# Kernel optimization log

Hardware: AMD Instinct MI355X
Metric: run time of the kernel (lower is better)

Reference implementation:

```python
import jax, jax.numpy as jnp
import numpy as np

DIM = 512
HEADS = 8
DIM_HEAD = 64
INNER = HEADS * DIM_HEAD
MAX_POS = 512


def setup_inputs() -> dict:
    key = jax.random.key(0)
    ks = jax.random.split(key, 6)
    b, n = 8, 1024
    x = jax.random.normal(ks[0], (b, n, DIM), dtype=jnp.float32)
    Wq = jax.random.normal(ks[1], (DIM, INNER), dtype=jnp.float32) * (DIM ** -0.5)
    Wkv = jax.random.normal(ks[2], (DIM, 2 * INNER), dtype=jnp.float32) * (DIM ** -0.5)
    rel_emb = jax.random.normal(ks[3], (2 * MAX_POS + 1, DIM_HEAD), dtype=jnp.float32) * 0.02
    Wo = jax.random.normal(ks[4], (INNER, DIM), dtype=jnp.float32) * (INNER ** -0.5)
    bo = jnp.zeros((DIM,), dtype=jnp.float32)
    return {"x": x, "Wq": Wq, "Wkv": Wkv, "rel_emb": rel_emb, "Wo": Wo, "bo": bo}


def reference(x, Wq, Wkv, rel_emb, Wo, bo):
    b, n, _ = x.shape
    scale = DIM_HEAD ** -0.5
    q = x @ Wq                      # [b, n, inner]
    kv = x @ Wkv                    # [b, n, 2*inner]
    k, v = jnp.split(kv, 2, axis=-1)
    # b n (h d) -> b h n d
    split_heads = lambda t: t.reshape(b, n, HEADS, DIM_HEAD).transpose(0, 2, 1, 3)
    q, k, v = split_heads(q), split_heads(k), split_heads(v)
    dots = jnp.einsum('bhid,bhjd->bhij', q, k) * scale  # [b,h,n,n]
    seq = jnp.arange(n)
    dist = jnp.clip(seq[:, None] - seq[None, :], -MAX_POS, MAX_POS) + MAX_POS  # [n,n]
    rel = rel_emb[dist]                                  # [n, n, d]
    pos_attn = jnp.einsum('bhnd,nrd->bhnr', q, rel) * scale
    dots = dots + pos_attn
    attn = jax.nn.softmax(dots, axis=-1)
    out = jnp.einsum('bhij,bhjd->bhid', attn, v)        # [b,h,n,d]
    out = out.transpose(0, 2, 1, 3).reshape(b, n, INNER)
    return out @ Wo + bo
```

## Files before the change

### kernel.cpp

```cpp
#include <hip/hip_runtime.h>

typedef __attribute__((ext_vector_type(8))) short bf16x8;
typedef __attribute__((ext_vector_type(4))) short bf16x4;
typedef __attribute__((ext_vector_type(4))) float f32x4;
typedef unsigned short u16;
typedef unsigned int u32;

#define MFMA16(a, b, c) __builtin_amdgcn_mfma_f32_16x16x32_bf16((a), (b), (c), 0, 0, 0)

__device__ __forceinline__ u16 f2b(float f) {
    u32 u = __float_as_uint(f);
    u32 r = u + 0x7fffu + ((u >> 16) & 1u);
    return (u16)(r >> 16);
}
__device__ __forceinline__ float b2f(u16 u) { return __uint_as_float(((u32)u) << 16); }
__device__ __forceinline__ u32 packbf(float lo, float hi) {
    return (u32)f2b(lo) | ((u32)f2b(hi) << 16);
}

__global__ void k_f32_to_bf16(const float* __restrict__ in, u16* __restrict__ out, int n) {
    int i = (blockIdx.x * blockDim.x + threadIdx.x) * 4;
    if (i + 3 < n) {
        float4 v = *(const float4*)(in + i);
        out[i] = f2b(v.x); out[i + 1] = f2b(v.y); out[i + 2] = f2b(v.z); out[i + 3] = f2b(v.w);
    } else {
        for (int j = i; j < n; ++j) out[j] = f2b(in[j]);
    }
}

__global__ void k_make_wqkv_t(const float* __restrict__ Wq, const float* __restrict__ Wkv,
                              u16* __restrict__ wt) {
    int tid = blockIdx.x * blockDim.x + threadIdx.x;
    int k = tid & 511, n = tid >> 9;
    float v = (n < 512) ? Wq[k * 512 + n] : Wkv[k * 1024 + (n - 512)];
    wt[n * 512 + k] = f2b(v);
}

__global__ void k_make_wo_t(const float* __restrict__ Wo, u16* __restrict__ wt) {
    int tid = blockIdx.x * blockDim.x + threadIdx.x;
    int k = tid & 511, n = tid >> 9;
    wt[n * 512 + k] = f2b(Wo[k * 512 + n]);
}

__global__ __launch_bounds__(256) void k_gemm_qkv(const u16* __restrict__ A, const u16* __restrict__ Bt,
                                                  u16* __restrict__ Q, u16* __restrict__ K,
                                                  u16* __restrict__ V) {
    __shared__ u16 As[128][40];
    __shared__ u16 Bs[128][40];
    const int t = threadIdx.x, l = t & 63, w = t >> 6;
    const int wr = w >> 1, wc = w & 1, l15 = l & 15, lg = l >> 4;
    const int m0 = blockIdx.x * 128, n0 = blockIdx.y * 128;
    f32x4 acc[4][4];
#pragma unroll
    for (int i = 0; i < 4; ++i)
#pragma unroll
        for (int j = 0; j < 4; ++j) acc[i][j] = (f32x4){0.f, 0.f, 0.f, 0.f};
    const int sr = t >> 1, sko = (t & 1) * 16;
    for (int k0 = 0; k0 < 512; k0 += 32) {
        __syncthreads();
        {
            const bf16x8* pa = (const bf16x8*)(A + (size_t)(m0 + sr) * 512 + k0 + sko);
            *(bf16x8*)&As[sr][sko] = pa[0];
            *(bf16x8*)&As[sr][sko + 8] = pa[1];
            const bf16x8* pb = (const bf16x8*)(Bt + (size_t)(n0 + sr) * 512 + k0 + sko);
            *(bf16x8*)&Bs[sr][sko] = pb[0];
            *(bf16x8*)&Bs[sr][sko + 8] = pb[1];
        }
        __syncthreads();
        bf16x8 af[4], bfr[4];
#pragma unroll
        for (int rt = 0; rt < 4; ++rt) af[rt] = *(const bf16x8*)&As[wr * 64 + rt * 16 + l15][lg * 8];
#pragma unroll
        for (int ct = 0; ct < 4; ++ct) bfr[ct] = *(const bf16x8*)&Bs[wc * 64 + ct * 16 + l15][lg * 8];
#pragma unroll
        for (int rt = 0; rt < 4; ++rt)
#pragma unroll
            for (int ct = 0; ct < 4; ++ct) acc[rt][ct] = MFMA16(af[rt], bfr[ct], acc[rt][ct]);
    }
#pragma unroll
    for (int rt = 0; rt < 4; ++rt)
#pragma unroll
        for (int ct = 0; ct < 4; ++ct) {
            int n = n0 + wc * 64 + ct * 16 + l15;
            int sec = n >> 9, nn = n & 511, h = nn >> 6, d = nn & 63;
            u16* dst = (sec == 0) ? Q : ((sec == 1) ? K : V);
#pragma unroll
            for (int r = 0; r < 4; ++r) {
                int m = m0 + wr * 64 + rt * 16 + lg * 4 + r;
                int b = m >> 10, pos = m & 1023, bh = b * 8 + h;
                dst[(size_t)bh * 65536 + (size_t)pos * 64 + d] = f2b(acc[rt][ct][r]);
            }
        }
}

__global__ __launch_bounds__(256) void k_transpose_v(const u16* __restrict__ V, u16* __restrict__ Vt) {
    __shared__ u16 tile[64][72];
    const int bh = blockIdx.x >> 4, pt = blockIdx.x & 15;
    const int p0 = pt * 64;
    const int t = threadIdx.x, r = t >> 2, c0 = (t & 3) * 16;
    const bf16x8* src = (const bf16x8*)(V + (size_t)bh * 65536 + (size_t)(p0 + r) * 64 + c0);
    *(bf16x8*)&tile[r][c0] = src[0];
    *(bf16x8*)&tile[r][c0 + 8] = src[1];
    __syncthreads();
    union { u16 u[8]; bf16x8 v; } o0, o1;
#pragma unroll
    for (int ii = 0; ii < 8; ++ii) {
        o0.u[ii] = tile[c0 + ii][r];
        o1.u[ii] = tile[c0 + 8 + ii][r];
    }
    bf16x8* dst = (bf16x8*)(Vt + (size_t)bh * 65536 + (size_t)r * 1024 + p0 + c0);
    dst[0] = o0.v;
    dst[1] = o1.v;
}

__global__ __launch_bounds__(512, 2) void k_attn(const u16* __restrict__ Q, const u16* __restrict__ K,
                                                 const u16* __restrict__ Vt, const u16* __restrict__ relb,
                                                 u16* __restrict__ Ob) {
    __shared__ u16 Ks[64][72];
    __shared__ u16 Vs[64][72];
    __shared__ u32 sdw[8][16][43];
    const int t = threadIdx.x, l = t & 63, w = t >> 6;
    const int l15 = l & 15, lg = l >> 4;
    const int g = (blockIdx.x & 7) * 64 + (blockIdx.x >> 3);
    const int bh = g >> 3;
    const int iw = (g & 7) * 128 + w * 16;
    const size_t hb = (size_t)bh * 65536;
    const int srow = t >> 3, scol = (t & 7) * 8;

    bf16x8 qf[2];
#pragma unroll
    for (int kf = 0; kf < 2; ++kf)
        qf[kf] = *(const bf16x8*)(Q + hb + (size_t)(iw + l15) * 64 + kf * 32 + lg * 8);

    f32x4 acc_o[4];
#pragma unroll
    for (int i = 0; i < 4; ++i) acc_o[i] = (f32x4){0.f, 0.f, 0.f, 0.f};
    float m_r = -1e30f, l_r = 0.f;

    bf16x8 kreg = *(const bf16x8*)(K + hb + (size_t)srow * 64 + scol);
    bf16x8 vreg = *(const bf16x8*)(Vt + hb + (size_t)srow * 1024 + scol);
    *(bf16x8*)&Ks[srow][scol] = kreg;
    *(bf16x8*)&Vs[srow][scol] = vreg;
    kreg = *(const bf16x8*)(K + hb + (size_t)(64 + srow) * 64 + scol);
    vreg = *(const bf16x8*)(Vt + hb + (size_t)srow * 1024 + 64 + scol);
    __syncthreads();

    for (int j0 = 0; j0 < 1024; j0 += 64) {
        f32x4 acc_s[4];
#pragma unroll
        for (int c = 0; c < 4; ++c) {
            acc_s[c] = (f32x4){0.f, 0.f, 0.f, 0.f};
#pragma unroll
            for (int kf = 0; kf < 2; ++kf) {
                bf16x8 kb = *(const bf16x8*)&Ks[c * 16 + l15][kf * 32 + lg * 8];
                acc_s[c] = MFMA16(kb, qf[kf], acc_s[c]);
            }
        }
        const int bd = iw - j0 - 63;
#pragma unroll
        for (int pt = 0; pt < 5; ++pt) {
            int dd = bd + pt * 16 + l15;
            dd = dd < -512 ? -512 : (dd > 512 ? 512 : dd);
            const u16* rrow = relb + (size_t)(dd + 512) * 64;
            f32x4 a = (f32x4){0.f, 0.f, 0.f, 0.f};
#pragma unroll
            for (int kf = 0; kf < 2; ++kf) {
                bf16x8 rb = *(const bf16x8*)(rrow + kf * 32 + lg * 8);
                a = MFMA16(rb, qf[kf], a);
            }
            int wc32 = pt * 8 + lg * 2;
            sdw[w][l15][wc32] = packbf(a[0], a[1]);
            sdw[w][l15][wc32 + 1] = packbf(a[2], a[3]);
        }
        asm volatile("s_waitcnt lgkmcnt(0)" ::: "memory");
        __builtin_amdgcn_sched_barrier(0);
        float sv[4][4];
#pragma unroll
        for (int c = 0; c < 4; ++c)
#pragma unroll
            for (int r = 0; r < 4; ++r) {
                int tt = l15 + 63 - c * 16 - lg * 4 - r;
                u32 wv = sdw[w][l15][tt >> 1];
                float band = b2f((u16)(wv >> ((tt & 1) * 16)));
                sv[c][r] = (acc_s[c][r] + band) * 0.125f;
            }
        float mt = sv[0][0];
#pragma unroll
        for (int c = 0; c < 4; ++c)
#pragma unroll
            for (int r = 0; r < 4; ++r) mt = fmaxf(mt, sv[c][r]);
        mt = fmaxf(mt, __shfl_xor(mt, 16, 64));
        mt = fmaxf(mt, __shfl_xor(mt, 32, 64));
        float mnew = fmaxf(m_r, mt);
        float alpha = __expf(m_r - mnew);
        m_r = mnew;
        float p[4][4];
        float rs = 0.f;
#pragma unroll
        for (int c = 0; c < 4; ++c)
#pragma unroll
            for (int r = 0; r < 4; ++r) {
                p[c][r] = __expf(sv[c][r] - mnew);
                rs += p[c][r];
            }
        rs += __shfl_xor(rs, 16, 64);
        rs += __shfl_xor(rs, 32, 64);
        l_r = l_r * alpha + rs;
#pragma unroll
        for (int dt = 0; dt < 4; ++dt)
#pragma unroll
            for (int r = 0; r < 4; ++r) acc_o[dt][r] *= alpha;
        union { u32 wd[4]; bf16x8 v; } pb[2];
#pragma unroll
        for (int kf = 0; kf < 2; ++kf)
#pragma unroll
            for (int h = 0; h < 4; ++h) {
                int c = kf * 2 + (h >> 1), r0 = (h & 1) * 2;
                pb[kf].wd[h] = packbf(p[c][r0], p[c][r0 + 1]);
            }
#pragma unroll
        for (int dt = 0; dt < 4; ++dt)
#pragma unroll
            for (int kf = 0; kf < 2; ++kf) {
                union { bf16x4 h[2]; bf16x8 v; } vb;
                vb.h[0] = *(const bf16x4*)&Vs[dt * 16 + l15][kf * 32 + lg * 4];
                vb.h[1] = *(const bf16x4*)&Vs[dt * 16 + l15][kf * 32 + 16 + lg * 4];
                acc_o[dt] = MFMA16(vb.v, pb[kf].v, acc_o[dt]);
            }
        __syncthreads();
        if (j0 + 64 < 1024) {
            *(bf16x8*)&Ks[srow][scol] = kreg;
            *(bf16x8*)&Vs[srow][scol] = vreg;
            int jp = j0 / 64 + 2;
            if (jp > 15) jp = 15;
            kreg = *(const bf16x8*)(K + hb + (size_t)(jp * 64 + srow) * 64 + scol);
            vreg = *(const bf16x8*)(Vt + hb + (size_t)srow * 1024 + jp * 64 + scol);
            __syncthreads();
        }
    }
    const int b = bh >> 3, h = bh & 7;
    const float rinv = 1.0f / l_r;
    const size_t rowbase = (size_t)(b * 1024 + iw + l15) * 512 + h * 64;
#pragma unroll
    for (int dt = 0; dt < 4; ++dt)
#pragma unroll
        for (int hp = 0; hp < 2; ++hp) {
            u32 pkd = packbf(acc_o[dt][hp * 2] * rinv, acc_o[dt][hp * 2 + 1] * rinv);
            *(u32*)(Ob + rowbase + dt * 16 + lg * 4 + hp * 2) = pkd;
        }
}

__global__ __launch_bounds__(256) void k_gemm_out(const u16* __restrict__ A, const u16* __restrict__ Bt,
                                                  const float* __restrict__ bias, float* __restrict__ out) {
    __shared__ u16 As[128][40];
    __shared__ u16 Bs[128][40];
    const int t = threadIdx.x, l = t & 63, w = t >> 6;
    const int wr = w >> 1, wc = w & 1, l15 = l & 15, lg = l >> 4;
    const int m0 = blockIdx.x * 128, n0 = blockIdx.y * 128;
    f32x4 acc[4][4];
#pragma unroll
    for (int i = 0; i < 4; ++i)
#pragma unroll
        for (int j = 0; j < 4; ++j) acc[i][j] = (f32x4){0.f, 0.f, 0.f, 0.f};
    const int sr = t >> 1, sko = (t & 1) * 16;
    for (int k0 = 0; k0 < 512; k0 += 32) {
        __syncthreads();
        {
            const bf16x8* pa = (const bf16x8*)(A + (size_t)(m0 + sr) * 512 + k0 + sko);
            *(bf16x8*)&As[sr][sko] = pa[0];
            *(bf16x8*)&As[sr][sko + 8] = pa[1];
            const bf16x8* pb = (const bf16x8*)(Bt + (size_t)(n0 + sr) * 512 + k0 + sko);
            *(bf16x8*)&Bs[sr][sko] = pb[0];
            *(bf16x8*)&Bs[sr][sko + 8] = pb[1];
        }
        __syncthreads();
        bf16x8 af[4], bfr[4];
#pragma unroll
        for (int rt = 0; rt < 4; ++rt) af[rt] = *(const bf16x8*)&As[wr * 64 + rt * 16 + l15][lg * 8];
#pragma unroll
        for (int ct = 0; ct < 4; ++ct) bfr[ct] = *(const bf16x8*)&Bs[wc * 64 + ct * 16 + l15][lg * 8];
#pragma unroll
        for (int rt = 0; rt < 4; ++rt)
#pragma unroll
            for (int ct = 0; ct < 4; ++ct) acc[rt][ct] = MFMA16(af[rt], bfr[ct], acc[rt][ct]);
    }
#pragma unroll
    for (int rt = 0; rt < 4; ++rt)
#pragma unroll
        for (int ct = 0; ct < 4; ++ct) {
            int n = n0 + wc * 64 + ct * 16 + l15;
            float bv = bias[n];
#pragma unroll
            for (int r = 0; r < 4; ++r) {
                int m = m0 + wr * 64 + rt * 16 + lg * 4 + r;
                out[(size_t)m * 512 + n] = acc[rt][ct][r] + bv;
            }
        }
}

extern "C" void kernel_launch(void* const* d_in, const int* in_sizes, int n_in,
                              void* d_out, int out_size, void* d_ws, size_t ws_size,
                              hipStream_t stream) {
    const float* x    = (const float*)d_in[0];
    const float* Wq   = (const float*)d_in[1];
    const float* Wkv  = (const float*)d_in[2];
    const float* rel  = (const float*)d_in[3];
    const float* Wo   = (const float*)d_in[4];
    const float* bo   = (const float*)d_in[5];
    float* out = (float*)d_out;
    char* ws = (char*)d_ws;

    u16* xb   = (u16*)(ws + 0);
    u16* wqkv = (u16*)(ws + 8388608);
    u16* wot  = (u16*)(ws + 9961472);
    u16* relb = (u16*)(ws + 10485760);
    u16* Q    = (u16*)(ws + 10616960);
    u16* K    = (u16*)(ws + 19005568);
    u16* V    = (u16*)(ws + 27394176);
    u16* Vt   = (u16*)(ws + 35782784);
    u16* Ob   = (u16*)(ws + 44171392);

    k_f32_to_bf16<<<4096, 256, 0, stream>>>(x, xb, 4194304);
    k_f32_to_bf16<<<65, 256, 0, stream>>>(rel, relb, 65600);
    k_make_wqkv_t<<<3072, 256, 0, stream>>>(Wq, Wkv, wqkv);
    k_make_wo_t<<<1024, 256, 0, stream>>>(Wo, wot);
    k_gemm_qkv<<<dim3(64, 12), 256, 0, stream>>>(xb, wqkv, Q, K, V);
    k_transpose_v<<<1024, 256, 0, stream>>>(V, Vt);
    k_attn<<<512, 512, 0, stream>>>(Q, K, Vt, relb, Ob);
    k_gemm_out<<<dim3(64, 4), 256, 0, stream>>>(Ob, wot, bo, out);
}
```

Before: 150.5 us.

## Split attention KV range in two with flash-decoding style combine kernel

Each attention block now processes only half of the key sequence, doubling the grid from 512 to 1024 blocks. Each block writes fp16 partial outputs plus per-row max and sum. A new combine kernel merges the two halves into the bf16 output layout. This targets low occupancy and load imbalance on the 256-CU device (512 blocks at 2 per CU), at the cost of extra partial-output traffic, an extra launch, and reuse of workspace buffers for the partials.

Result: slower. 188.7 us (+25.4%).

```diff
diff --git a/kernel.cpp b/kernel.cpp
--- a/kernel.cpp
+++ b/kernel.cpp
@@ -1,4 +1,5 @@
 #include <hip/hip_runtime.h>
+#include <hip/hip_fp16.h>
 
 typedef __attribute__((ext_vector_type(8))) short bf16x8;
 typedef __attribute__((ext_vector_type(4))) short bf16x4;
@@ -17,6 +18,10 @@
 __device__ __forceinline__ u32 packbf(float lo, float hi) {
     return (u32)f2b(lo) | ((u32)f2b(hi) << 16);
 }
+__device__ __forceinline__ u32 packh(float lo, float hi) {
+    return (u32)__half_as_ushort(__float2half(lo)) | ((u32)__half_as_ushort(__float2half(hi)) << 16);
+}
+__device__ __forceinline__ float h2f(u16 u) { return __half2float(__ushort_as_half(u)); }
 
 __global__ void k_f32_to_bf16(const float* __restrict__ in, u16* __restrict__ out, int n) {
     int i = (blockIdx.x * blockDim.x + threadIdx.x) * 4;
@@ -115,15 +120,18 @@
 
 __global__ __launch_bounds__(512, 2) void k_attn(const u16* __restrict__ Q, const u16* __restrict__ K,
                                                  const u16* __restrict__ Vt, const u16* __restrict__ relb,
-                                                 u16* __restrict__ Ob) {
+                                                 u16* __restrict__ Op0, u16* __restrict__ Op1,
+                                                 float* __restrict__ ml) {
     __shared__ u16 Ks[64][72];
     __shared__ u16 Vs[64][72];
-    __shared__ u32 sdw[8][16][43];
+    __shared__ u32 sdw[8][16][41];
     const int t = threadIdx.x, l = t & 63, w = t >> 6;
     const int l15 = l & 15, lg = l >> 4;
-    const int g = (blockIdx.x & 7) * 64 + (blockIdx.x >> 3);
-    const int bh = g >> 3;
-    const int iw = (g & 7) * 128 + w * 16;
+    const int g2 = (blockIdx.x & 7) * 128 + (blockIdx.x >> 3);
+    const int bh = g2 >> 4;
+    const int iw = ((g2 >> 1) & 7) * 128 + w * 16;
+    const int split = g2 & 1;
+    const int jbase = split * 512;
     const size_t hb = (size_t)bh * 65536;
     const int srow = t >> 3, scol = (t & 7) * 8;
 
@@ -137,15 +145,16 @@
     for (int i = 0; i < 4; ++i) acc_o[i] = (f32x4){0.f, 0.f, 0.f, 0.f};
     float m_r = -1e30f, l_r = 0.f;
 
-    bf16x8 kreg = *(const bf16x8*)(K + hb + (size_t)srow * 64 + scol);
-    bf16x8 vreg = *(const bf16x8*)(Vt + hb + (size_t)srow * 1024 + scol);
+    bf16x8 kreg = *(const bf16x8*)(K + hb + (size_t)(jbase + srow) * 64 + scol);
+    bf16x8 vreg = *(const bf16x8*)(Vt + hb + (size_t)srow * 1024 + jbase + scol);
     *(bf16x8*)&Ks[srow][scol] = kreg;
     *(bf16x8*)&Vs[srow][scol] = vreg;
-    kreg = *(const bf16x8*)(K + hb + (size_t)(64 + srow) * 64 + scol);
-    vreg = *(const bf16x8*)(Vt + hb + (size_t)srow * 1024 + 64 + scol);
+    kreg = *(const bf16x8*)(K + hb + (size_t)(jbase + 64 + srow) * 64 + scol);
+    vreg = *(const bf16x8*)(Vt + hb + (size_t)srow * 1024 + jbase + 64 + scol);
     __syncthreads();
 
-    for (int j0 = 0; j0 < 1024; j0 += 64) {
+    for (int it = 0; it < 8; ++it) {
+        const int j0 = jbase + it * 64;
         f32x4 acc_s[4];
 #pragma unroll
         for (int c = 0; c < 4; ++c) {
@@ -228,26 +237,53 @@
                 acc_o[dt] = MFMA16(vb.v, pb[kf].v, acc_o[dt]);
             }
         __syncthreads();
-        if (j0 + 64 < 1024) {
+        if (it < 7) {
             *(bf16x8*)&Ks[srow][scol] = kreg;
             *(bf16x8*)&Vs[srow][scol] = vreg;
-            int jp = j0 / 64 + 2;
-            if (jp > 15) jp = 15;
-            kreg = *(const bf16x8*)(K + hb + (size_t)(jp * 64 + srow) * 64 + scol);
-            vreg = *(const bf16x8*)(Vt + hb + (size_t)srow * 1024 + jp * 64 + scol);
+            int jp = (it + 2 < 8) ? it + 2 : 7;
+            kreg = *(const bf16x8*)(K + hb + (size_t)(jbase + jp * 64 + srow) * 64 + scol);
+            vreg = *(const bf16x8*)(Vt + hb + (size_t)srow * 1024 + jbase + jp * 64 + scol);
             __syncthreads();
         }
     }
-    const int b = bh >> 3, h = bh & 7;
+    u16* Op = split ? Op1 : Op0;
     const float rinv = 1.0f / l_r;
-    const size_t rowbase = (size_t)(b * 1024 + iw + l15) * 512 + h * 64;
-#pragma unroll
-    for (int dt = 0; dt < 4; ++dt)
-#pragma unroll
-        for (int hp = 0; hp < 2; ++hp) {
-            u32 pkd = packbf(acc_o[dt][hp * 2] * rinv, acc_o[dt][hp * 2 + 1] * rinv);
-            *(u32*)(Ob + rowbase + dt * 16 + lg * 4 + hp * 2) = pkd;
-        }
+    const size_t obase = hb + (size_t)(iw + l15) * 64;
+#pragma unroll
+    for (int dt = 0; dt < 4; ++dt) {
+        u32* d = (u32*)(Op + obase + dt * 16 + lg * 4);
+        d[0] = packh(acc_o[dt][0] * rinv, acc_o[dt][1] * rinv);
+        d[1] = packh(acc_o[dt][2] * rinv, acc_o[dt][3] * rinv);
+    }
+    if (lg == 0) {
+        float2 mlv = make_float2(m_r, l_r);
+        *(float2*)(ml + ((size_t)split * 65536 + (size_t)bh * 1024 + iw + l15) * 2) = mlv;
+    }
+}
+
+__global__ __launch_bounds__(256) void k_combine(const u16* __restrict__ Op0, const u16* __restrict__ Op1,
+                                                 const float* __restrict__ ml, u16* __restrict__ Ob) {
+    int tid = blockIdx.x * 256 + threadIdx.x;
+    int row = tid >> 3, oct = tid & 7;
+    int bh = row >> 10, pos = row & 1023;
+    float m0 = ml[(size_t)row * 2], l0 = ml[(size_t)row * 2 + 1];
+    float m1 = ml[(size_t)(65536 + row) * 2], l1 = ml[(size_t)(65536 + row) * 2 + 1];
+    float M = fmaxf(m0, m1);
+    float a0 = l0 * __expf(m0 - M), a1 = l1 * __expf(m1 - M);
+    float inv = 1.0f / (a0 + a1);
+    float w0 = a0 * inv, w1 = a1 * inv;
+    size_t src = (size_t)row * 64 + oct * 8;
+    const u32* p0 = (const u32*)(Op0 + src);
+    const u32* p1 = (const u32*)(Op1 + src);
+    int b = bh >> 3, h = bh & 7;
+    u32* dst = (u32*)(Ob + (size_t)(b * 1024 + pos) * 512 + h * 64 + oct * 8);
+#pragma unroll
+    for (int q = 0; q < 4; ++q) {
+        u32 x0 = p0[q], x1 = p1[q];
+        float lo = w0 * h2f((u16)x0) + w1 * h2f((u16)x1);
+        float hi = w0 * h2f((u16)(x0 >> 16)) + w1 * h2f((u16)(x1 >> 16));
+        dst[q] = packbf(lo, hi);
+    }
 }
 
 __global__ __launch_bounds__(256) void k_gemm_out(const u16* __restrict__ A, const u16* __restrict__ Bt,
@@ -310,15 +346,18 @@
     float* out = (float*)d_out;
     char* ws = (char*)d_ws;
 
-    u16* xb   = (u16*)(ws + 0);
-    u16* wqkv = (u16*)(ws + 8388608);
-    u16* wot  = (u16*)(ws + 9961472);
-    u16* relb = (u16*)(ws + 10485760);
-    u16* Q    = (u16*)(ws + 10616960);
-    u16* K    = (u16*)(ws + 19005568);
-    u16* V    = (u16*)(ws + 27394176);
-    u16* Vt   = (u16*)(ws + 35782784);
-    u16* Ob   = (u16*)(ws + 44171392);
+    u16*   wot  = (u16*)(ws + 0x0000000);
+    u16*   relb = (u16*)(ws + 0x0080000);
+    u16*   Q    = (u16*)(ws + 0x0100000);
+    u16*   K    = (u16*)(ws + 0x0900000);
+    u16*   Vt   = (u16*)(ws + 0x1100000);
+    u16*   Ob   = (u16*)(ws + 0x1900000);
+    u16*   xb   = (u16*)(ws + 0x2100000);
+    u16*   wqkv = (u16*)(ws + 0x2900000);
+    u16*   V    = (u16*)(ws + 0x2B00000);
+    u16*   Op0  = xb;
+    float* mlws = (float*)wqkv;
+    u16*   Op1  = V;
 
     k_f32_to_bf16<<<4096, 256, 0, stream>>>(x, xb, 4194304);
     k_f32_to_bf16<<<65, 256, 0, stream>>>(rel, relb, 65600);
@@ -326,6 +365,7 @@
     k_make_wo_t<<<1024, 256, 0, stream>>>(Wo, wot);
     k_gemm_qkv<<<dim3(64, 12), 256, 0, stream>>>(xb, wqkv, Q, K, V);
     k_transpose_v<<<1024, 256, 0, stream>>>(V, Vt);
-    k_attn<<<512, 512, 0, stream>>>(Q, K, Vt, relb, Ob);
+    k_attn<<<1024, 512, 0, stream>>>(Q, K, Vt, relb, Op0, Op1, mlws);
+    k_combine<<<2048, 256, 0, stream>>>(Op0, Op1, mlws, Ob);
     k_gemm_out<<<dim3(64, 4), 256, 0, stream>>>(Ob, wot, bo, out);
 }
```
